# Kernel optimization log

Measured on AMD Instinct MI355X. Metric: run time of the kernel, lower is better.

## Reference

```python
import jax, jax.numpy as jnp
import numpy as np
import math

EMB, SEQ, OUT, FF, B = 1024, 1024, 2, 1024, 32
EPS = 1e-5


def _build_pe(seq_len, emb_dim):
    # Faithful to the buggy torch loop: for even i, pe[pos,i] is first set to sin
    # then immediately overwritten by cos(pos / 10000**(2*(i+1)/emb_dim));
    # odd indices are never written (stay 0).
    pos = np.arange(seq_len, dtype=np.float64)[:, None]
    i = np.arange(0, emb_dim, 2, dtype=np.float64)[None, :]
    pe = np.zeros((seq_len, emb_dim), dtype=np.float32)
    pe[:, ::2] = np.cos(pos / 10000.0 ** (2.0 * (i + 1.0) / emb_dim)).astype(np.float32)
    return jnp.asarray(pe)[None]  # [1, S, D]


def setup_inputs() -> dict:
    key = jax.random.key(0)
    ks = jax.random.split(key, 24)
    std = 0.02
    W = lambda k, o, i: jax.random.normal(k, (o, i), jnp.float32) * std
    b = lambda k, o: jax.random.normal(k, (o,), jnp.float32) * std
    return {
        "x": jax.random.normal(ks[0], (B, SEQ, EMB), jnp.float32),
        "pe": _build_pe(SEQ, EMB),
        "ln1_g": jnp.ones((EMB,), jnp.float32), "ln1_b": jnp.zeros((EMB,), jnp.float32),
        "Wq": W(ks[1], EMB, EMB), "bq": b(ks[2], EMB),
        "Wk": W(ks[3], EMB, EMB), "bk": b(ks[4], EMB),
        "Wv": W(ks[5], EMB, EMB), "bv": b(ks[6], EMB),
        "Wo": W(ks[7], EMB, EMB), "bo": b(ks[8], EMB),
        "ln2_g": jnp.ones((EMB,), jnp.float32), "ln2_b": jnp.zeros((EMB,), jnp.float32),
        "W1": W(ks[9], FF, EMB), "b1": b(ks[10], FF),
        "W2": W(ks[11], EMB, FF), "b2": b(ks[12], EMB),
        "Wc": W(ks[13], OUT, EMB), "bc": b(ks[14], OUT),
    }


def _ln(x, g, bias):
    mu = jnp.mean(x, axis=-1, keepdims=True)
    var = jnp.mean(jnp.square(x - mu), axis=-1, keepdims=True)
    return (x - mu) * jax.lax.rsqrt(var + EPS) * g + bias


def _block(x, ln1_g, ln1_b, Wq, bq, Wk, bk, Wv, bv, Wo, bo, ln2_g, ln2_b, W1, b1, W2, b2):
    h = _ln(x, ln1_g, ln1_b)
    q = h @ Wq.T + bq
    k = h @ Wk.T + bk
    v = h @ Wv.T + bv
    scores = jnp.einsum('bqd,bkd->bqk', q, k) / math.sqrt(EMB)
    w = jax.nn.softmax(scores, axis=-1)  # [B,S,S]
    attn = jnp.einsum('bqk,bkd->bqd', w, v) @ Wo.T + bo
    x2 = x + attn  # dropout is identity in eval
    h2 = _ln(x2, ln2_g, ln2_b)
    ff = jax.nn.relu(h2 @ W1.T + b1) @ W2.T + b2
    return x2 + ff, w


def reference(x, pe, ln1_g, ln1_b, Wq, bq, Wk, bk, Wv, bv, Wo, bo, ln2_g, ln2_b, W1, b1, W2, b2, Wc, bc):
    x1 = math.sqrt(EMB) * x + pe
    # Original forward applies block net2_1 twice (net2_2 is unused) -> reuse params.
    p = (ln1_g, ln1_b, Wq, bq, Wk, bk, Wv, bv, Wo, bo, ln2_g, ln2_b, W1, b1, W2, b2)
    x2_1, w1 = _block(x1, *p)
    x2_2, w2 = _block(x2_1, *p)
    logits = x2_2[:, 0, :] @ Wc.T + bc
    return logits, w1, w2
```

## Files before the change

### kernel.cpp

```cpp
#include <hip/hip_runtime.h>
#include <cstdint>


#define AS1 __attribute__((address_space(1)))
#define AS3 __attribute__((address_space(3)))

typedef __attribute__((ext_vector_type(8))) short bf16x8;
typedef __attribute__((ext_vector_type(4))) float f32x4;
typedef __attribute__((ext_vector_type(4))) unsigned short us4;

__device__ __forceinline__ unsigned short f2bf(float f) {
  unsigned int u = __builtin_bit_cast(unsigned int, f);
  u += 0x7fffu + ((u >> 16) & 1u);
  return (unsigned short)(u >> 16);
}

__device__ __forceinline__ void gload_lds16(const void* g, void* l) {
  auto gp = reinterpret_cast<AS1 unsigned int*>(reinterpret_cast<uintptr_t>(g));
  auto lp = reinterpret_cast<AS3 unsigned int*>(reinterpret_cast<uintptr_t>(l));
  __builtin_amdgcn_global_load_lds(gp, lp, 16, 0, 0);
}

enum { M_BF16 = 0, M_RELU = 1, M_VT = 2, M_SCORES = 3, M_RESID = 4 };

template<int MODE>
__global__ __launch_bounds__(256, 2) void gemm_bt(
    const unsigned short* __restrict__ A, long long sAb,
    const unsigned short* __restrict__ B, long long sBb,
    const float* __restrict__ bias,
    const float* __restrict__ resid,
    float* __restrict__ outF,
    unsigned short* __restrict__ outBF,
    long long sOb, int N, int K, float scale)
{
  __shared__ __align__(16) unsigned short As[128 * 64];
  __shared__ __align__(16) unsigned short Bs[128 * 64];
  const int t    = threadIdx.x;
  const int w    = t >> 6;
  const int lane = t & 63;
  const int quad = lane >> 4;
  const int l16  = lane & 15;
  const int bz   = blockIdx.z;
  const unsigned short* Ab = A + (long long)bz * sAb;
  const unsigned short* Bb = B + (long long)bz * sBb;
  const int m0 = blockIdx.y * 128;
  const int n0 = blockIdx.x * 128;
  const int srow = t >> 3;
  const int scol = (t & 7) * 8;
  const int wr = (w >> 1) * 64;
  const int wc = (w & 1) * 64;

  const f32x4 zero = {0.f, 0.f, 0.f, 0.f};
  f32x4 acc[4][4];
#pragma unroll
  for (int i = 0; i < 4; ++i)
#pragma unroll
    for (int j = 0; j < 4; ++j) acc[i][j] = zero;

  for (int k0 = 0; k0 < K; k0 += 64) {
#pragma unroll
    for (int c = 0; c < 4; ++c) {
      gload_lds16(Ab + (long long)(m0 + c * 32 + srow) * K + (k0 + scol),
                  As + c * 2048 + w * 512);
      gload_lds16(Bb + (long long)(n0 + c * 32 + srow) * K + (k0 + scol),
                  Bs + c * 2048 + w * 512);
    }
    __syncthreads();
#pragma unroll
    for (int kk = 0; kk < 64; kk += 32) {
      bf16x8 af[4], bfr[4];
#pragma unroll
      for (int i = 0; i < 4; ++i)
        af[i] = *(const bf16x8*)&As[(wr + i * 16 + l16) * 64 + kk + quad * 8];
#pragma unroll
      for (int j = 0; j < 4; ++j)
        bfr[j] = *(const bf16x8*)&Bs[(wc + j * 16 + l16) * 64 + kk + quad * 8];
#pragma unroll
      for (int i = 0; i < 4; ++i)
#pragma unroll
        for (int j = 0; j < 4; ++j)
          acc[i][j] = __builtin_amdgcn_mfma_f32_16x16x32_bf16(af[i], bfr[j], acc[i][j], 0, 0, 0);
    }
    __syncthreads();
  }

#pragma unroll
  for (int i = 0; i < 4; ++i) {
#pragma unroll
    for (int j = 0; j < 4; ++j) {
      const int mt = m0 + wr + i * 16 + quad * 4;
      const int nt = n0 + wc + j * 16 + l16;
      f32x4 d = acc[i][j];
      if (MODE == M_BF16 || MODE == M_RELU) {
        const float bv = bias ? bias[nt] : 0.0f;
#pragma unroll
        for (int r = 0; r < 4; ++r) {
          float v = d[r] + bv;
          if (MODE == M_RELU) v = fmaxf(v, 0.0f);
          outBF[(long long)bz * sOb + (long long)(mt + r) * N + nt] = f2bf(v);
        }
      } else if (MODE == M_SCORES) {
#pragma unroll
        for (int r = 0; r < 4; ++r)
          outF[(long long)bz * sOb + (long long)(mt + r) * N + nt] = d[r] * scale;
      } else if (MODE == M_RESID) {
        const float bv = bias[nt];
#pragma unroll
        for (int r = 0; r < 4; ++r) {
          const long long idx = (long long)(mt + r) * N + nt;
          outF[idx] = resid[idx] + d[r] + bv;
        }
      } else if (MODE == M_VT) {
        const float bv = bias[nt];
        us4 pk;
#pragma unroll
        for (int r = 0; r < 4; ++r) pk[r] = f2bf(d[r] + bv);
        const int b = mt >> 10;
        const int s = mt & 1023;
        *(us4*)&outBF[(long long)b * 1048576 + (long long)nt * 1024 + s] = pk;
      }
    }
  }
}

template<int EMBED>
__global__ __launch_bounds__(256) void ln_kernel(
    const float* __restrict__ xin, const float* __restrict__ pe,
    float* __restrict__ x1out,
    const float* __restrict__ g, const float* __restrict__ bb,
    unsigned short* __restrict__ hout)
{
  __shared__ float red[8];
  const long long row = blockIdx.x;
  const int t = threadIdx.x, lane = t & 63, w = t >> 6;
  float4 v = *(const float4*)(xin + row * 1024 + t * 4);
  if (EMBED) {
    const int s = (int)(row & 1023);
    float4 p = *(const float4*)(pe + (long long)s * 1024 + t * 4);
    v.x = 32.0f * v.x + p.x;
    v.y = 32.0f * v.y + p.y;
    v.z = 32.0f * v.z + p.z;
    v.w = 32.0f * v.w + p.w;
    *(float4*)(x1out + row * 1024 + t * 4) = v;
  }
  float sum = v.x + v.y + v.z + v.w;
  float sq  = v.x * v.x + v.y * v.y + v.z * v.z + v.w * v.w;
#pragma unroll
  for (int off = 32; off > 0; off >>= 1) {
    sum += __shfl_down(sum, off, 64);
    sq  += __shfl_down(sq,  off, 64);
  }
  if (lane == 0) { red[w] = sum; red[4 + w] = sq; }
  __syncthreads();
  sum = red[0] + red[1] + red[2] + red[3];
  sq  = red[4] + red[5] + red[6] + red[7];
  const float mu  = sum * (1.0f / 1024.0f);
  const float var = sq * (1.0f / 1024.0f) - mu * mu;
  const float rs  = rsqrtf(var + 1e-5f);
  float4 gg = *(const float4*)(g + t * 4);
  float4 bv = *(const float4*)(bb + t * 4);
  us4 h;
  h[0] = f2bf((v.x - mu) * rs * gg.x + bv.x);
  h[1] = f2bf((v.y - mu) * rs * gg.y + bv.y);
  h[2] = f2bf((v.z - mu) * rs * gg.z + bv.z);
  h[3] = f2bf((v.w - mu) * rs * gg.w + bv.w);
  *(us4*)(hout + row * 1024 + t * 4) = h;
}

__global__ __launch_bounds__(256) void softmax_kernel(
    float* __restrict__ wio, unsigned short* __restrict__ wbf)
{
  __shared__ float red[8];
  const long long row = blockIdx.x;
  const int t = threadIdx.x, lane = t & 63, w = t >> 6;
  float* p = wio + row * 1024 + t * 4;
  float4 v = *(const float4*)p;
  float mx = fmaxf(fmaxf(v.x, v.y), fmaxf(v.z, v.w));
#pragma unroll
  for (int off = 32; off > 0; off >>= 1) mx = fmaxf(mx, __shfl_down(mx, off, 64));
  if (lane == 0) red[w] = mx;
  __syncthreads();
  mx = fmaxf(fmaxf(red[0], red[1]), fmaxf(red[2], red[3]));
  __syncthreads();
  const float e0 = __expf(v.x - mx), e1 = __expf(v.y - mx);
  const float e2 = __expf(v.z - mx), e3 = __expf(v.w - mx);
  float s = e0 + e1 + e2 + e3;
#pragma unroll
  for (int off = 32; off > 0; off >>= 1) s += __shfl_down(s, off, 64);
  if (lane == 0) red[w] = s;
  __syncthreads();
  s = red[0] + red[1] + red[2] + red[3];
  const float inv = 1.0f / s;
  float4 o; o.x = e0 * inv; o.y = e1 * inv; o.z = e2 * inv; o.w = e3 * inv;
  *(float4*)p = o;
  us4 ob;
  ob[0] = f2bf(o.x); ob[1] = f2bf(o.y); ob[2] = f2bf(o.z); ob[3] = f2bf(o.w);
  *(us4*)(wbf + row * 1024 + t * 4) = ob;
}

__global__ __launch_bounds__(256) void cvt_bf16_kernel(
    const float* __restrict__ src, unsigned short* __restrict__ dst, int n4)
{
  const int i = blockIdx.x * 256 + threadIdx.x;
  if (i < n4) {
    float4 v = *(const float4*)(src + (long long)i * 4);
    us4 o;
    o[0] = f2bf(v.x); o[1] = f2bf(v.y); o[2] = f2bf(v.z); o[3] = f2bf(v.w);
    *(us4*)(dst + (long long)i * 4) = o;
  }
}

__global__ __launch_bounds__(256) void logits_kernel(
    const float* __restrict__ x, const float* __restrict__ Wc,
    const float* __restrict__ bc, float* __restrict__ out)
{
  __shared__ float red[4];
  const int blk = blockIdx.x;
  const int b = blk >> 1, o = blk & 1;
  const int t = threadIdx.x, lane = t & 63, w = t >> 6;
  const float* xr = x + (long long)b * 1048576;
  const float* wr = Wc + o * 1024;
  float4 xv = *(const float4*)(xr + t * 4);
  float4 wv = *(const float4*)(wr + t * 4);
  float s = xv.x * wv.x + xv.y * wv.y + xv.z * wv.z + xv.w * wv.w;
#pragma unroll
  for (int off = 32; off > 0; off >>= 1) s += __shfl_down(s, off, 64);
  if (lane == 0) red[w] = s;
  __syncthreads();
  if (t == 0) out[blk] = red[0] + red[1] + red[2] + red[3] + bc[o];
}

extern "C" void kernel_launch(void* const* d_in, const int* in_sizes, int n_in,
                              void* d_out, int out_size, void* d_ws, size_t ws_size,
                              hipStream_t stream)
{
  const float* x    = (const float*)d_in[0];
  const float* pe   = (const float*)d_in[1];
  const float* ln1g = (const float*)d_in[2];
  const float* ln1b = (const float*)d_in[3];
  const float* Wq   = (const float*)d_in[4];
  const float* bq   = (const float*)d_in[5];
  const float* Wk   = (const float*)d_in[6];
  const float* bk   = (const float*)d_in[7];
  const float* Wv   = (const float*)d_in[8];
  const float* bv   = (const float*)d_in[9];
  const float* Wo   = (const float*)d_in[10];
  const float* bo   = (const float*)d_in[11];
  const float* ln2g = (const float*)d_in[12];
  const float* ln2b = (const float*)d_in[13];
  const float* W1   = (const float*)d_in[14];
  const float* b1   = (const float*)d_in[15];
  const float* W2   = (const float*)d_in[16];
  const float* b2   = (const float*)d_in[17];
  const float* Wc   = (const float*)d_in[18];
  const float* bc   = (const float*)d_in[19];
  float* out = (float*)d_out;

  char* ws = (char*)d_ws;
  float*          xbuf  = (float*)ws;
  unsigned short* h_bf  = (unsigned short*)(ws + 134217728LL);
  unsigned short* q_bf  = (unsigned short*)(ws + 134217728LL + 1*67108864LL);
  unsigned short* k_bf  = (unsigned short*)(ws + 134217728LL + 2*67108864LL);
  unsigned short* vT_bf = (unsigned short*)(ws + 134217728LL + 3*67108864LL);
  unsigned short* wts   = (unsigned short*)(ws + 134217728LL + 4*67108864LL);
  unsigned short* Wq_bf = wts + 0LL * 1048576;
  unsigned short* Wk_bf = wts + 1LL * 1048576;
  unsigned short* Wv_bf = wts + 2LL * 1048576;
  unsigned short* Wo_bf = wts + 3LL * 1048576;
  unsigned short* W1_bf = wts + 4LL * 1048576;
  unsigned short* W2_bf = wts + 5LL * 1048576;
  unsigned short* attn_bf = q_bf;
  unsigned short* w_bf    = k_bf;
  unsigned short* ff1_bf  = vT_bf;

  const dim3 blk(256);
  cvt_bf16_kernel<<<1024, blk, 0, stream>>>(Wq, Wq_bf, 262144);
  cvt_bf16_kernel<<<1024, blk, 0, stream>>>(Wk, Wk_bf, 262144);
  cvt_bf16_kernel<<<1024, blk, 0, stream>>>(Wv, Wv_bf, 262144);
  cvt_bf16_kernel<<<1024, blk, 0, stream>>>(Wo, Wo_bf, 262144);
  cvt_bf16_kernel<<<1024, blk, 0, stream>>>(W1, W1_bf, 262144);
  cvt_bf16_kernel<<<1024, blk, 0, stream>>>(W2, W2_bf, 262144);

  const dim3 gProj(8, 256, 1);
  const dim3 gAttn(8, 8, 32);

  for (int blkI = 0; blkI < 2; ++blkI) {
    float* wslot = out + 64 + (long long)blkI * 33554432LL;

    if (blkI == 0)
      ln_kernel<1><<<32768, blk, 0, stream>>>(x, pe, xbuf, ln1g, ln1b, h_bf);
    else
      ln_kernel<0><<<32768, blk, 0, stream>>>(xbuf, nullptr, nullptr, ln1g, ln1b, h_bf);

    gemm_bt<M_BF16><<<gProj, blk, 0, stream>>>(h_bf, 0, Wq_bf, 0, bq, nullptr,
                                               nullptr, q_bf, 0, 1024, 1024, 1.0f);
    gemm_bt<M_BF16><<<gProj, blk, 0, stream>>>(h_bf, 0, Wk_bf, 0, bk, nullptr,
                                               nullptr, k_bf, 0, 1024, 1024, 1.0f);
    gemm_bt<M_VT><<<gProj, blk, 0, stream>>>(h_bf, 0, Wv_bf, 0, bv, nullptr,
                                             nullptr, vT_bf, 0, 1024, 1024, 1.0f);

    gemm_bt<M_SCORES><<<gAttn, blk, 0, stream>>>(q_bf, 1048576, k_bf, 1048576, nullptr,
                                                 nullptr, wslot, nullptr, 1048576,
                                                 1024, 1024, 0.03125f);
    softmax_kernel<<<32768, blk, 0, stream>>>(wslot, w_bf);

    gemm_bt<M_BF16><<<gAttn, blk, 0, stream>>>(w_bf, 1048576, vT_bf, 1048576, nullptr,
                                               nullptr, nullptr, attn_bf, 1048576,
                                               1024, 1024, 1.0f);
    gemm_bt<M_RESID><<<gProj, blk, 0, stream>>>(attn_bf, 0, Wo_bf, 0, bo, xbuf,
                                                xbuf, nullptr, 0, 1024, 1024, 1.0f);

    ln_kernel<0><<<32768, blk, 0, stream>>>(xbuf, nullptr, nullptr, ln2g, ln2b, h_bf);
    gemm_bt<M_RELU><<<gProj, blk, 0, stream>>>(h_bf, 0, W1_bf, 0, b1, nullptr,
                                               nullptr, ff1_bf, 0, 1024, 1024, 1.0f);
    gemm_bt<M_RESID><<<gProj, blk, 0, stream>>>(ff1_bf, 0, W2_bf, 0, b2, xbuf,
                                                xbuf, nullptr, 0, 1024, 1024, 1.0f);
  }

  logits_kernel<<<64, blk, 0, stream>>>(xbuf, Wc, bc, out);
  (void)in_sizes; (void)n_in; (void)out_size; (void)ws_size;
}
```

Baseline: 2.344 ms.

## Fuse QKV projections, store scores as bf16, merge weight prep kernels

Concatenates Wq/Wk/Wv into one bf16 weight and bias buffer so a single GEMM over N=3072 writes Q, K and transposed V. Score GEMM output is written as bf16 into a scratch buffer instead of fp32 into the output slot, and softmax reads bf16 and writes the fp32 weights. This halves score write/read traffic. The six weight conversions are merged into one launch. Occupancy hint is raised to 3 blocks per CU. Rounding scores to bf16 before softmax reduces precision.

```diff
diff --git a/kernel.cpp b/kernel.cpp
--- a/kernel.cpp
+++ b/kernel.cpp
@@ -14,6 +14,9 @@
   u += 0x7fffu + ((u >> 16) & 1u);
   return (unsigned short)(u >> 16);
 }
+__device__ __forceinline__ float bf2f(unsigned short h) {
+  return __builtin_bit_cast(float, (unsigned int)h << 16);
+}
 
 __device__ __forceinline__ void gload_lds16(const void* g, void* l) {
   auto gp = reinterpret_cast<AS1 unsigned int*>(reinterpret_cast<uintptr_t>(g));
@@ -21,10 +24,10 @@
   __builtin_amdgcn_global_load_lds(gp, lp, 16, 0, 0);
 }
 
-enum { M_BF16 = 0, M_RELU = 1, M_VT = 2, M_SCORES = 3, M_RESID = 4 };
+enum { M_BF16 = 0, M_RELU = 1, M_QKV = 2, M_SCBF = 3, M_RESID = 4 };
 
 template<int MODE>
-__global__ __launch_bounds__(256, 2) void gemm_bt(
+__global__ __launch_bounds__(256, 3) void gemm_bt(
     const unsigned short* __restrict__ A, long long sAb,
     const unsigned short* __restrict__ B, long long sBb,
     const float* __restrict__ bias,
@@ -99,10 +102,10 @@
           if (MODE == M_RELU) v = fmaxf(v, 0.0f);
           outBF[(long long)bz * sOb + (long long)(mt + r) * N + nt] = f2bf(v);
         }
-      } else if (MODE == M_SCORES) {
+      } else if (MODE == M_SCBF) {
 #pragma unroll
         for (int r = 0; r < 4; ++r)
-          outF[(long long)bz * sOb + (long long)(mt + r) * N + nt] = d[r] * scale;
+          outBF[(long long)bz * sOb + (long long)(mt + r) * N + nt] = f2bf(d[r] * scale);
       } else if (MODE == M_RESID) {
         const float bv = bias[nt];
 #pragma unroll
@@ -110,14 +113,24 @@
           const long long idx = (long long)(mt + r) * N + nt;
           outF[idx] = resid[idx] + d[r] + bv;
         }
-      } else if (MODE == M_VT) {
+      } else if (MODE == M_QKV) {
+        const int seg = n0 >> 10;
+        const int ntl = nt - (seg << 10);
         const float bv = bias[nt];
-        us4 pk;
-#pragma unroll
-        for (int r = 0; r < 4; ++r) pk[r] = f2bf(d[r] + bv);
-        const int b = mt >> 10;
-        const int s = mt & 1023;
-        *(us4*)&outBF[(long long)b * 1048576 + (long long)nt * 1024 + s] = pk;
+        if (seg < 2) {
+          unsigned short* dst = outBF + (long long)seg * 33554432LL;
+#pragma unroll
+          for (int r = 0; r < 4; ++r)
+            dst[(long long)(mt + r) * 1024 + ntl] = f2bf(d[r] + bv);
+        } else {
+          unsigned short* dst = outBF + 2LL * 33554432LL;
+          us4 pk;
+#pragma unroll
+          for (int r = 0; r < 4; ++r) pk[r] = f2bf(d[r] + bv);
+          const int b = mt >> 10;
+          const int s = mt & 1023;
+          *(us4*)&dst[(long long)b * 1048576 + (long long)ntl * 1024 + s] = pk;
+        }
       }
     }
   }
@@ -168,13 +181,15 @@
 }
 
 __global__ __launch_bounds__(256) void softmax_kernel(
-    float* __restrict__ wio, unsigned short* __restrict__ wbf)
+    const unsigned short* __restrict__ sbf,
+    float* __restrict__ wout, unsigned short* __restrict__ wbf)
 {
   __shared__ float red[8];
   const long long row = blockIdx.x;
   const int t = threadIdx.x, lane = t & 63, w = t >> 6;
-  float* p = wio + row * 1024 + t * 4;
-  float4 v = *(const float4*)p;
+  us4 sv = *(const us4*)(sbf + row * 1024 + t * 4);
+  float4 v;
+  v.x = bf2f(sv[0]); v.y = bf2f(sv[1]); v.z = bf2f(sv[2]); v.w = bf2f(sv[3]);
   float mx = fmaxf(fmaxf(v.x, v.y), fmaxf(v.z, v.w));
 #pragma unroll
   for (int off = 32; off > 0; off >>= 1) mx = fmaxf(mx, __shfl_down(mx, off, 64));
@@ -192,22 +207,44 @@
   s = red[0] + red[1] + red[2] + red[3];
   const float inv = 1.0f / s;
   float4 o; o.x = e0 * inv; o.y = e1 * inv; o.z = e2 * inv; o.w = e3 * inv;
-  *(float4*)p = o;
+  *(float4*)(wout + row * 1024 + t * 4) = o;
   us4 ob;
   ob[0] = f2bf(o.x); ob[1] = f2bf(o.y); ob[2] = f2bf(o.z); ob[3] = f2bf(o.w);
   *(us4*)(wbf + row * 1024 + t * 4) = ob;
 }
 
-__global__ __launch_bounds__(256) void cvt_bf16_kernel(
-    const float* __restrict__ src, unsigned short* __restrict__ dst, int n4)
-{
-  const int i = blockIdx.x * 256 + threadIdx.x;
-  if (i < n4) {
-    float4 v = *(const float4*)(src + (long long)i * 4);
-    us4 o;
-    o[0] = f2bf(v.x); o[1] = f2bf(v.y); o[2] = f2bf(v.z); o[3] = f2bf(v.w);
-    *(us4*)(dst + (long long)i * 4) = o;
-  }
+__global__ __launch_bounds__(256) void prep_kernel(
+    const float* __restrict__ Wq, const float* __restrict__ Wk, const float* __restrict__ Wv,
+    const float* __restrict__ Wo, const float* __restrict__ W1, const float* __restrict__ W2,
+    const float* __restrict__ bq, const float* __restrict__ bk, const float* __restrict__ bv,
+    unsigned short* __restrict__ qkvw, unsigned short* __restrict__ Wo_bf,
+    unsigned short* __restrict__ W1_bf, unsigned short* __restrict__ W2_bf,
+    float* __restrict__ qkvb)
+{
+  const int y = blockIdx.y;
+  const long long i = blockIdx.x * 256 + threadIdx.x;
+  if (y == 6) {
+    if (i < 768) {
+      const float* src = (i < 256) ? bq : (i < 512) ? bk : bv;
+      float4 v = *(const float4*)(src + (i & 255) * 4);
+      *(float4*)(qkvb + i * 4) = v;
+    }
+    return;
+  }
+  const float* src;
+  unsigned short* dst;
+  switch (y) {
+    case 0: src = Wq; dst = qkvw;            break;
+    case 1: src = Wk; dst = qkvw + 1048576;  break;
+    case 2: src = Wv; dst = qkvw + 2097152;  break;
+    case 3: src = Wo; dst = Wo_bf;           break;
+    case 4: src = W1; dst = W1_bf;           break;
+    default: src = W2; dst = W2_bf;          break;
+  }
+  float4 v = *(const float4*)(src + i * 4);
+  us4 o;
+  o[0] = f2bf(v.x); o[1] = f2bf(v.y); o[2] = f2bf(v.z); o[3] = f2bf(v.w);
+  *(us4*)(dst + i * 4) = o;
 }
 
 __global__ __launch_bounds__(256) void logits_kernel(
@@ -259,28 +296,25 @@
   char* ws = (char*)d_ws;
   float*          xbuf  = (float*)ws;
   unsigned short* h_bf  = (unsigned short*)(ws + 134217728LL);
-  unsigned short* q_bf  = (unsigned short*)(ws + 134217728LL + 1*67108864LL);
-  unsigned short* k_bf  = (unsigned short*)(ws + 134217728LL + 2*67108864LL);
-  unsigned short* vT_bf = (unsigned short*)(ws + 134217728LL + 3*67108864LL);
-  unsigned short* wts   = (unsigned short*)(ws + 134217728LL + 4*67108864LL);
-  unsigned short* Wq_bf = wts + 0LL * 1048576;
-  unsigned short* Wk_bf = wts + 1LL * 1048576;
-  unsigned short* Wv_bf = wts + 2LL * 1048576;
-  unsigned short* Wo_bf = wts + 3LL * 1048576;
-  unsigned short* W1_bf = wts + 4LL * 1048576;
-  unsigned short* W2_bf = wts + 5LL * 1048576;
+  unsigned short* q_bf  = (unsigned short*)(ws + 134217728LL + 1 * 67108864LL);
+  unsigned short* k_bf  = (unsigned short*)(ws + 134217728LL + 2 * 67108864LL);
+  unsigned short* vT_bf = (unsigned short*)(ws + 134217728LL + 3 * 67108864LL);
+  unsigned short* wts   = (unsigned short*)(ws + 134217728LL + 4 * 67108864LL);
+  unsigned short* QKV_bf = wts;
+  unsigned short* Wo_bf  = wts + 3LL * 1048576;
+  unsigned short* W1_bf  = wts + 4LL * 1048576;
+  unsigned short* W2_bf  = wts + 5LL * 1048576;
+  float*          qkvb   = (float*)(wts + 6LL * 1048576);
+  unsigned short* sc_bf   = h_bf;
+  unsigned short* w_bf    = k_bf;
   unsigned short* attn_bf = q_bf;
-  unsigned short* w_bf    = k_bf;
   unsigned short* ff1_bf  = vT_bf;
 
   const dim3 blk(256);
-  cvt_bf16_kernel<<<1024, blk, 0, stream>>>(Wq, Wq_bf, 262144);
-  cvt_bf16_kernel<<<1024, blk, 0, stream>>>(Wk, Wk_bf, 262144);
-  cvt_bf16_kernel<<<1024, blk, 0, stream>>>(Wv, Wv_bf, 262144);
-  cvt_bf16_kernel<<<1024, blk, 0, stream>>>(Wo, Wo_bf, 262144);
-  cvt_bf16_kernel<<<1024, blk, 0, stream>>>(W1, W1_bf, 262144);
-  cvt_bf16_kernel<<<1024, blk, 0, stream>>>(W2, W2_bf, 262144);
-
+  prep_kernel<<<dim3(1024, 7), blk, 0, stream>>>(Wq, Wk, Wv, Wo, W1, W2, bq, bk, bv,
+                                                 QKV_bf, Wo_bf, W1_bf, W2_bf, qkvb);
+
+  const dim3 gQKV(24, 256, 1);
   const dim3 gProj(8, 256, 1);
   const dim3 gAttn(8, 8, 32);
 
@@ -292,17 +326,13 @@
     else
       ln_kernel<0><<<32768, blk, 0, stream>>>(xbuf, nullptr, nullptr, ln1g, ln1b, h_bf);
 
-    gemm_bt<M_BF16><<<gProj, blk, 0, stream>>>(h_bf, 0, Wq_bf, 0, bq, nullptr,
-                                               nullptr, q_bf, 0, 1024, 1024, 1.0f);
-    gemm_bt<M_BF16><<<gProj, blk, 0, stream>>>(h_bf, 0, Wk_bf, 0, bk, nullptr,
-                                               nullptr, k_bf, 0, 1024, 1024, 1.0f);
-    gemm_bt<M_VT><<<gProj, blk, 0, stream>>>(h_bf, 0, Wv_bf, 0, bv, nullptr,
-                                             nullptr, vT_bf, 0, 1024, 1024, 1.0f);
-
-    gemm_bt<M_SCORES><<<gAttn, blk, 0, stream>>>(q_bf, 1048576, k_bf, 1048576, nullptr,
-                                                 nullptr, wslot, nullptr, 1048576,
-                                                 1024, 1024, 0.03125f);
-    softmax_kernel<<<32768, blk, 0, stream>>>(wslot, w_bf);
+    gemm_bt<M_QKV><<<gQKV, blk, 0, stream>>>(h_bf, 0, QKV_bf, 0, qkvb, nullptr,
+                                             nullptr, q_bf, 0, 3072, 1024, 1.0f);
+
+    gemm_bt<M_SCBF><<<gAttn, blk, 0, stream>>>(q_bf, 1048576, k_bf, 1048576, nullptr,
+                                               nullptr, nullptr, sc_bf, 1048576,
+                                               1024, 1024, 0.03125f);
+    softmax_kernel<<<32768, blk, 0, stream>>>(sc_bf, wslot, w_bf);
 
     gemm_bt<M_BF16><<<gAttn, blk, 0, stream>>>(w_bf, 1048576, vT_bf, 1048576, nullptr,
                                                nullptr, nullptr, attn_bf, 1048576,
```

New measurement: 2.245 ms. 1.04x faster.
